# Kernel tuning notes

Measured on AMD Instinct MI355X. Metric: run time of the kernel, lower is better.

Reference implementation:

```python
import jax, jax.numpy as jnp
import numpy as np

MAX_RES = 5.0  # max_residue_magnitude
DG = 16       # deform_groups
KH = KW = 3
K = KH * KW
PAD = 1
STRIDE = 1
DIL = 1


def conv3x3(x, w, b):
    y = jax.lax.conv_general_dilated(
        x, w, window_strides=(1, 1), padding='SAME',
        dimension_numbers=('NCHW', 'OIHW', 'NCHW'))
    return y + b[None, :, None, None]


def lrelu(x):
    return jnp.where(x >= 0, x, 0.1 * x)


def deform_conv2d(x, offset, mask, weight, bias):
    # x: [B,C,H,W]; offset: [B,2*DG*K,Ho,Wo]; mask: [B,DG*K,Ho,Wo]
    B, C, H, W = x.shape
    Cout = weight.shape[0]
    Ho = (H + 2 * PAD - DIL * (KH - 1) - 1) // STRIDE + 1
    Wo = (W + 2 * PAD - DIL * (KW - 1) - 1) // STRIDE + 1
    Cg = C // DG

    # torchvision layout: offset channel = g*(2*K) + 2*k + {0:y, 1:x}
    off = offset.reshape(B, DG, K, 2, Ho, Wo)
    oy, ox = off[:, :, :, 0], off[:, :, :, 1]           # [B,DG,K,Ho,Wo]
    msk = mask.reshape(B, DG, K, Ho, Wo)

    ki = DIL * (jnp.arange(K) // KW)                    # [K] kernel row offsets
    kj = DIL * (jnp.arange(K) % KW)
    base_y = STRIDE * jnp.arange(Ho) - PAD              # [Ho]
    base_x = STRIDE * jnp.arange(Wo) - PAD              # [Wo]
    py = base_y[None, None, None, :, None] + ki[None, None, :, None, None] + oy
    px = base_x[None, None, None, None, :] + kj[None, None, :, None, None] + ox

    xg = x.reshape(B, DG, Cg, H * W)

    y0 = jnp.floor(py)
    x0 = jnp.floor(px)
    wy1 = py - y0
    wx1 = px - x0

    def corner(iy, ix, w_c):
        valid = ((iy >= 0) & (iy <= H - 1) & (ix >= 0) & (ix <= W - 1)).astype(x.dtype)
        iyc = jnp.clip(iy, 0, H - 1).astype(jnp.int32)
        ixc = jnp.clip(ix, 0, W - 1).astype(jnp.int32)
        idx = (iyc * W + ixc).reshape(B, DG, 1, K * Ho * Wo)
        g = jnp.take_along_axis(
            xg, jnp.broadcast_to(idx, (B, DG, Cg, K * Ho * Wo)), axis=3)
        g = g.reshape(B, DG, Cg, K, Ho, Wo)
        return g * (w_c * valid)[:, :, None]

    val = (corner(y0, x0, (1 - wy1) * (1 - wx1))
           + corner(y0, x0 + 1, (1 - wy1) * wx1)
           + corner(y0 + 1, x0, wy1 * (1 - wx1))
           + corner(y0 + 1, x0 + 1, wy1 * wx1))

    val = val * msk[:, :, None]                          # modulation
    val = val.reshape(B, C, K, Ho, Wo)                   # columns
    out = jnp.einsum('bckhw,ock->bohw', val, weight.reshape(Cout, C, K))
    return out + bias[None, :, None, None]


def setup_inputs() -> dict:
    key = jax.random.key(0)
    ks = jax.random.split(key, 12)
    B, H, W = 1, 192, 192
    inp = {
        'x':    jax.random.normal(ks[0], (B, 128, H, W), jnp.float32),
        'cond': jax.random.normal(ks[1], (B, 192, H, W), jnp.float32),
        'weight': jax.random.normal(ks[2], (64, 128, 3, 3), jnp.float32) * 0.03,
        'bias':   jax.random.normal(ks[3], (64,), jnp.float32) * 0.01,
        'w1': jax.random.normal(ks[4], (64, 192, 3, 3), jnp.float32) * 0.03,
        'b1': jax.random.normal(ks[5], (64,), jnp.float32) * 0.01,
        'w2': jax.random.normal(ks[6], (64, 64, 3, 3), jnp.float32) * 0.05,
        'b2': jax.random.normal(ks[7], (64,), jnp.float32) * 0.01,
        'w3': jax.random.normal(ks[8], (64, 64, 3, 3), jnp.float32) * 0.05,
        'b3': jax.random.normal(ks[9], (64,), jnp.float32) * 0.01,
        'w4': jax.random.normal(ks[10], (432, 64, 3, 3), jnp.float32) * 0.05,
        'b4': jax.random.normal(ks[11], (432,), jnp.float32) * 0.01,
    }
    return inp


def reference(x, cond, weight, bias, w1, b1, w2, b2, w3, b3, w4, b4):
    h = lrelu(conv3x3(cond, w1, b1))
    h = lrelu(conv3x3(h, w2, b2))
    h = lrelu(conv3x3(h, w3, b3))
    out = conv3x3(h, w4, b4)                       # [B, 27*DG, H, W]
    offset, mask = out[:, :18 * DG], out[:, 18 * DG:]
    offset = MAX_RES * jnp.tanh(offset)
    mask = jax.nn.sigmoid(mask)
    return deform_conv2d(x, offset, mask, weight, bias)
```

## Files before the change

kernel.cpp:

```cpp
#include <hip/hip_runtime.h>
#include <hip/hip_bf16.h>
#include <math.h>

#define IMG_H 192
#define IMG_W 192
#define NPIX (IMG_H * IMG_W)
#define PADW 194
#define PPIX (PADW * PADW)
#define PH 208
#define PW 208

typedef _Float16 h8 __attribute__((ext_vector_type(8)));
typedef _Float16 h4 __attribute__((ext_vector_type(4)));
typedef float f32x4 __attribute__((ext_vector_type(4)));

__device__ __forceinline__ float act_tanh5(float x) {
    const float t = __expf(2.f * x);
    return 5.f * (t - 1.f) / (t + 1.f);
}
__device__ __forceinline__ float act_sig(float x) {
    return 1.f / (1.f + __expf(-x));
}

typedef __attribute__((address_space(1))) const unsigned int GU32;
typedef __attribute__((address_space(3))) unsigned int LU32;
__device__ __forceinline__ void cp16(const void* g, void* l) {
    __builtin_amdgcn_global_load_lds((GU32*)g, (LU32*)l, 16, 0, 0);
}

__global__ __launch_bounds__(256) void cond_pack_k(
    const float* __restrict__ src, _Float16* __restrict__ dst)
{
    const int y = blockIdx.x;
    const int c = blockIdx.y;
    const int x = threadIdx.x;
    if (x >= PADW) return;
    const bool inb = (y >= 1 && y <= IMG_H && x >= 1 && x <= IMG_W);
    h8 v[4];
#pragma unroll
    for (int j = 0; j < 32; j++)
        ((_Float16*)v)[j] = inb
            ? (_Float16)src[(size_t)(c * 32 + j) * NPIX + (y - 1) * IMG_W + (x - 1)]
            : (_Float16)0.f;
    h8* d = (h8*)&dst[((size_t)c * PPIX + (size_t)y * PADW + x) * 32];
    d[0] = v[0]; d[1] = v[1]; d[2] = v[2]; d[3] = v[3];
}

template<int CIN, int COP, int COUT>
__device__ __forceinline__ void pack_body(
    int bx, const float* __restrict__ src, _Float16* __restrict__ dst)
{
    const int chunk = bx / 9, k = bx % 9;
    for (int i = threadIdx.x; i < COP * 32; i += 256) {
        const int co = i >> 5, cil = i & 31;
        float v = 0.f;
        if (co < COUT)
            v = src[((size_t)(co * CIN + chunk * 32 + cil)) * 9 + k];
        dst[(size_t)bx * COP * 32 + i] = (_Float16)v;
    }
}

__global__ __launch_bounds__(256) void pack_all_w_k(
    const float* __restrict__ w1, const float* __restrict__ w2,
    const float* __restrict__ w3, const float* __restrict__ w4,
    _Float16* __restrict__ wp1, _Float16* __restrict__ wp2,
    _Float16* __restrict__ wp3, _Float16* __restrict__ wp4)
{
    const int b = blockIdx.x;
    if      (b < 54) pack_body<192, 64, 64>(b, w1, wp1);
    else if (b < 72) pack_body<64, 64, 64>(b - 54, w2, wp2);
    else if (b < 90) pack_body<64, 64, 64>(b - 72, w3, wp3);
    else             pack_body<64, 448, 432>(b - 90, w4, wp4);
}

__global__ __launch_bounds__(192) void xg_pack_k(
    const float* __restrict__ x, _Float16* __restrict__ xg)
{
    const int y  = blockIdx.x;
    const int dg = blockIdx.y;
    const int xc = threadIdx.x;
    h8 v;
#pragma unroll
    for (int chl = 0; chl < 8; chl++)
        v[chl] = (_Float16)x[(size_t)(dg * 8 + chl) * NPIX + y * IMG_W + xc];
    *(h8*)&xg[(((size_t)dg * PH + y + 6) * PW + xc + 6) * 8] = v;
}

__global__ __launch_bounds__(256) void wdg_pack_k(
    const float* __restrict__ w, _Float16* __restrict__ wdg)
{
    const int i = blockIdx.x * 256 + threadIdx.x;
    if (i >= 16 * 64 * 96) return;
    const int ks = i % 96;
    const int rest = i / 96;
    const int co = rest % 64;
    const int dg = rest / 64;
    const int k = ks >> 3, chl = ks & 7;
    float v = 0.f;
    if (ks < 72)
        v = w[((size_t)co * 128 + dg * 8 + chl) * 9 + k];
    wdg[i] = (_Float16)v;
}

template<int CHUNKS, int ACT, int COP, int T8>
__global__ __launch_bounds__(256) void conv_lds_k(
    const _Float16* __restrict__ in,
    const _Float16* __restrict__ wpk,
    const float* __restrict__ bias,
    _Float16* __restrict__ out)
{
    constexpr int HALO = T8 ? 10 : 18;
    constexpr int NF   = T8 ? 1 : 4;
    constexpr int TDIM = T8 ? 24 : 12;
    constexpr int TSZ  = T8 ? 8 : 16;
    constexpr int INU  = HALO * HALO * 4;
    constexpr int ROWU = HALO * 4;

    __shared__ _Float16 in_lds[HALO * HALO * 32];
    __shared__ _Float16 w_lds[9 * 64 * 32];

    const int t    = threadIdx.x;
    const int lane = t & 63;
    const int wv   = __builtin_amdgcn_readfirstlane(t >> 6);
    const int col  = lane & 15;
    const int quad = lane >> 4;
    const int bx   = blockIdx.x;
    const int tx0  = (bx % TDIM) * TSZ;
    const int ty0  = (bx / TDIM) * TSZ;
    const int cobase = blockIdx.y * 64;

    f32x4 acc[4][NF];
#pragma unroll
    for (int m = 0; m < 4; m++)
#pragma unroll
        for (int s = 0; s < NF; s++) {
            f32x4 z = {0.f, 0.f, 0.f, 0.f};
            acc[m][s] = z;
        }

    for (int c = 0; c < CHUNKS; c++) {
        __syncthreads();
        {
            const char* gbase = (const char*)in + (size_t)c * PPIX * 64;
            char* lbase = (char*)in_lds + (size_t)wv * 64 * 16;
#pragma unroll
            for (int i = 0; i < (INU + 255) / 256; i++) {
                const int j = t + i * 256;
                if (j < INU) {
                    const int row = j / ROWU;
                    const int u   = j - row * ROWU;
                    cp16(gbase + ((size_t)(ty0 + row) * PADW + tx0) * 64 + u * 16,
                         lbase + (size_t)i * 256 * 16);
                }
            }
        }
        {
            const char* gw = (const char*)wpk
                + ((size_t)(c * 9) * COP + cobase) * 64 + t * 16;
            char* lw = (char*)w_lds + (size_t)wv * 64 * 16;
#pragma unroll
            for (int k = 0; k < 9; k++)
                cp16(gw + (size_t)k * COP * 64, lw + k * 4096);
        }
        __syncthreads();

#pragma unroll
        for (int k = 0; k < 9; k++) {
            const int ky = k / 3, kx = k % 3;
            h8 af[4];
#pragma unroll
            for (int m = 0; m < 4; m++)
                af[m] = *(const h8*)&w_lds[(k * 64 + m * 16 + col) * 32 + quad * 8];
            h8 bf[NF];
            if (T8) {
                bf[0] = *(const h8*)&in_lds[
                    ((2 * wv + (col >> 3) + ky) * HALO + (col & 7) + kx) * 32 + quad * 8];
            } else {
#pragma unroll
                for (int s = 0; s < NF; s++)
                    bf[s] = *(const h8*)&in_lds[
                        ((4 * wv + s + ky) * HALO + col + kx) * 32 + quad * 8];
            }
#pragma unroll
            for (int m = 0; m < 4; m++)
#pragma unroll
                for (int s = 0; s < NF; s++)
                    acc[m][s] = __builtin_amdgcn_mfma_f32_16x16x32_f16(
                        af[m], bf[s], acc[m][s], 0, 0, 0);
        }
    }

#pragma unroll
    for (int m = 0; m < 4; m++) {
#pragma unroll
        for (int s = 0; s < NF; s++) {
            int gy, gx;
            if (T8) { gy = ty0 + 2 * wv + (col >> 3); gx = tx0 + (col & 7); }
            else    { gy = ty0 + 4 * wv + s;          gx = tx0 + col; }
            const int ca = cobase + m * 16 + quad * 4;
            if (ACT == 1) {
                h4 st;
#pragma unroll
                for (int r = 0; r < 4; r++) {
                    float v = acc[m][s][r] + bias[ca + r];
                    st[r] = (_Float16)((v >= 0.f) ? v : 0.1f * v);
                }
                *(h4*)&out[((size_t)(ca >> 5) * PPIX + (size_t)(gy + 1) * PADW + (gx + 1)) * 32
                           + (ca & 31)] = st;
            } else {
#pragma unroll
                for (int r = 0; r < 4; r++) {
                    const int co = ca + r;
                    if (co < 432)
                        out[(size_t)co * NPIX + (size_t)gy * IMG_W + gx] =
                            (_Float16)(acc[m][s][r] + bias[co]);
                }
            }
        }
    }
}

__global__ __launch_bounds__(256) void deform_mfma_k(
    const _Float16* __restrict__ xg,
    const _Float16* __restrict__ od,
    const _Float16* __restrict__ wdg,
    const float* __restrict__ bias,
    float* __restrict__ out)
{
    __shared__ __align__(16) _Float16 val4[4][32][104];

    const int t    = threadIdx.x;
    const int lane = t & 63;
    const int wv   = __builtin_amdgcn_readfirstlane(t >> 6);
    const int col  = lane & 15;
    const int quad = lane >> 4;
    const int bx   = blockIdx.x;
    const int gy   = bx / 6;
    const int gx0  = (bx % 6) * 32;
    const int pixrow = gy * IMG_W + gx0;

    for (int i = t; i < 4 * 32 * 4; i += 256) {
        const int dgl = i >> 7;
        const int r   = i & 127;
        const int px  = r >> 2;
        const int j   = r & 3;
        h8 z = {0, 0, 0, 0, 0, 0, 0, 0};
        *(h8*)&val4[dgl][px][72 + 8 * j] = z;
    }

    f32x4 acc[2];
    {
        f32x4 z = {0.f, 0.f, 0.f, 0.f};
        acc[0] = z; acc[1] = z;
    }

    for (int dq = 0; dq < 4; dq++) {
        __syncthreads();
        for (int idx = t; idx < 1152; idx += 256) {
            const int pxl  = idx & 31;
            const int rest = idx >> 5;
            const int k    = rest % 9;
            const int dgl  = rest / 9;
            const int dg   = dq * 4 + dgl;
            const int kc   = dg * 9 + k;
            const int pix  = pixrow + pxl;
            const float oy = act_tanh5((float)od[(size_t)(2 * kc) * NPIX + pix]);
            const float ox = act_tanh5((float)od[(size_t)(2 * kc + 1) * NPIX + pix]);
            const float m  = act_sig((float)od[(size_t)(288 + kc) * NPIX + pix]);
            const float py  = (float)(gy - 1 + k / 3) + oy;
            const float pxx = (float)(gx0 + pxl - 1 + k % 3) + ox;
            const float y0 = floorf(py), x0 = floorf(pxx);
            const float fy = py - y0, fx = pxx - x0;
            const int iy = (int)y0 + 6, ix = (int)x0 + 6;
            const _Float16* p = xg + (((size_t)dg * PH + iy) * PW + ix) * 8;
            const h8 c00 = *(const h8*)p;
            const h8 c01 = *(const h8*)(p + 8);
            const h8 c10 = *(const h8*)(p + PW * 8);
            const h8 c11 = *(const h8*)(p + PW * 8 + 8);
            const float ey = 1.f - fy, ex = 1.f - fx;
            const _Float16 s00 = (_Float16)(ey * ex * m);
            const _Float16 s01 = (_Float16)(ey * fx * m);
            const _Float16 s10 = (_Float16)(fy * ex * m);
            const _Float16 s11 = (_Float16)(fy * fx * m);
            const h8 v = c00 * s00 + c01 * s01 + c10 * s10 + c11 * s11;
            *(h8*)&val4[dgl][pxl][k * 8] = v;
        }
        __syncthreads();

#pragma unroll
        for (int dgl = 0; dgl < 4; dgl++) {
            const int dg = dq * 4 + dgl;
            const _Float16* wbase = wdg + ((size_t)dg * 64 + wv * 16 + col) * 96;
#pragma unroll
            for (int ks = 0; ks < 3; ks++) {
                const h8 a  = *(const h8*)(wbase + ks * 32 + quad * 8);
                const h8 b0 = *(const h8*)&val4[dgl][col][ks * 32 + quad * 8];
                const h8 b1 = *(const h8*)&val4[dgl][16 + col][ks * 32 + quad * 8];
                acc[0] = __builtin_amdgcn_mfma_f32_16x16x32_f16(a, b0, acc[0], 0, 0, 0);
                acc[1] = __builtin_amdgcn_mfma_f32_16x16x32_f16(a, b1, acc[1], 0, 0, 0);
            }
        }
    }

    const int co = wv * 16 + quad * 4;
#pragma unroll
    for (int n = 0; n < 2; n++) {
        const int gx = gx0 + n * 16 + col;
#pragma unroll
        for (int r = 0; r < 4; r++)
            out[(size_t)(co + r) * NPIX + gy * IMG_W + gx] = acc[n][r] + bias[co + r];
    }
}

extern "C" void kernel_launch(void* const* d_in, const int* in_sizes, int n_in,
                              void* d_out, int out_size, void* d_ws, size_t ws_size,
                              hipStream_t stream) {
    (void)in_sizes; (void)n_in; (void)out_size; (void)ws_size;

    const float* x      = (const float*)d_in[0];
    const float* cond   = (const float*)d_in[1];
    const float* weight = (const float*)d_in[2];
    const float* bias   = (const float*)d_in[3];
    const float* w1     = (const float*)d_in[4];
    const float* b1     = (const float*)d_in[5];
    const float* w2     = (const float*)d_in[6];
    const float* b2     = (const float*)d_in[7];
    const float* w3     = (const float*)d_in[8];
    const float* b3     = (const float*)d_in[9];
    const float* w4     = (const float*)d_in[10];
    const float* b4     = (const float*)d_in[11];
    float* out = (float*)d_out;

    char* ws = (char*)d_ws;
    size_t off = 0;
    auto take = [&](size_t bytes) -> char* {
        char* p = ws + off;
        off = (off + bytes + 255) & ~(size_t)255;
        return p;
    };
    _Float16* act_cond = (_Float16*)take((size_t)6 * PPIX * 32 * 2);
    _Float16* pb_all   = (_Float16*)take((size_t)3 * 2 * PPIX * 32 * 2);
    _Float16* pb1 = pb_all;
    _Float16* pb2 = pb1 + (size_t)2 * PPIX * 32;
    _Float16* pb3 = pb2 + (size_t)2 * PPIX * 32;
    _Float16* od  = (_Float16*)take((size_t)432 * NPIX * 2);
    _Float16* wp1 = (_Float16*)take((size_t)54 * 64 * 32 * 2);
    _Float16* wp2 = (_Float16*)take((size_t)18 * 64 * 32 * 2);
    _Float16* wp3 = (_Float16*)take((size_t)18 * 64 * 32 * 2);
    _Float16* wp4 = (_Float16*)take((size_t)18 * 448 * 32 * 2);
    _Float16* xg  = (_Float16*)take((size_t)16 * PH * PW * 8 * 2);
    _Float16* wdg = (_Float16*)take((size_t)16 * 64 * 96 * 2);

    hipMemsetAsync(pb_all, 0, (size_t)3 * 2 * PPIX * 32 * 2, stream);
    hipMemsetAsync(xg,     0, (size_t)16 * PH * PW * 8 * 2, stream);

    hipLaunchKernelGGL(cond_pack_k, dim3(PADW, 6), dim3(256), 0, stream, cond, act_cond);
    hipLaunchKernelGGL(pack_all_w_k, dim3(108), dim3(256), 0, stream,
                       w1, w2, w3, w4, wp1, wp2, wp3, wp4);
    hipLaunchKernelGGL(xg_pack_k,  dim3(192, 16), dim3(192), 0, stream, x, xg);
    hipLaunchKernelGGL(wdg_pack_k, dim3((16 * 64 * 96 + 255) / 256), dim3(256), 0, stream, weight, wdg);

    hipLaunchKernelGGL((conv_lds_k<6, 1, 64, 1>),  dim3(576, 1), dim3(256), 0, stream, act_cond, wp1, b1, pb1);
    hipLaunchKernelGGL((conv_lds_k<2, 1, 64, 1>),  dim3(576, 1), dim3(256), 0, stream, pb1, wp2, b2, pb2);
    hipLaunchKernelGGL((conv_lds_k<2, 1, 64, 1>),  dim3(576, 1), dim3(256), 0, stream, pb2, wp3, b3, pb3);
    hipLaunchKernelGGL((conv_lds_k<2, 2, 448, 0>), dim3(144, 7), dim3(256), 0, stream, pb3, wp4, b4, od);
    hipLaunchKernelGGL(deform_mfma_k, dim3(1152), dim3(256), 0, stream, xg, od, wdg, bias, out);
}
```

Baseline: 259.6 us.

## Batch deform sampling into two 8-group chunks with staged loads for memory-level parallelism

The deformable-conv kernel now handles 8 deform groups per chunk (2 chunks instead of 4), doubling the shared val buffer. The sampling loop is split into three fully unrolled phases: issue all offset/mask loads, compute the bilinear coordinates, then issue all corner gathers. This exposes more outstanding memory requests per thread and halves the number of barriers. The cost is more registers and LDS, partly bounded by launch_bounds(256,3), with a risk of spills or lower occupancy.

```diff
diff --git a/kernel.cpp b/kernel.cpp
--- a/kernel.cpp
+++ b/kernel.cpp
@@ -220,14 +220,14 @@
     }
 }
 
-__global__ __launch_bounds__(256) void deform_mfma_k(
+__global__ __launch_bounds__(256, 3) void deform_mfma_k(
     const _Float16* __restrict__ xg,
     const _Float16* __restrict__ od,
     const _Float16* __restrict__ wdg,
     const float* __restrict__ bias,
     float* __restrict__ out)
 {
-    __shared__ __align__(16) _Float16 val4[4][32][104];
+    __shared__ __align__(16) _Float16 val4[8][32][104];
 
     const int t    = threadIdx.x;
     const int lane = t & 63;
@@ -239,7 +239,7 @@
     const int gx0  = (bx % 6) * 32;
     const int pixrow = gy * IMG_W + gx0;
 
-    for (int i = t; i < 4 * 32 * 4; i += 256) {
+    for (int i = t; i < 8 * 32 * 4; i += 256) {
         const int dgl = i >> 7;
         const int r   = i & 127;
         const int px  = r >> 2;
@@ -254,42 +254,71 @@
         acc[0] = z; acc[1] = z;
     }
 
-    for (int dq = 0; dq < 4; dq++) {
+    for (int ch = 0; ch < 2; ch++) {
         __syncthreads();
-        for (int idx = t; idx < 1152; idx += 256) {
-            const int pxl  = idx & 31;
-            const int rest = idx >> 5;
+
+        _Float16 ry[9], rx[9], rm[9];
+#pragma unroll
+        for (int u = 0; u < 9; u++) {
+            const int id   = t + (u << 8);
+            const int pxl  = id & 31;
+            const int rest = id >> 5;
             const int k    = rest % 9;
             const int dgl  = rest / 9;
-            const int dg   = dq * 4 + dgl;
-            const int kc   = dg * 9 + k;
+            const int kc   = (ch * 8 + dgl) * 9 + k;
             const int pix  = pixrow + pxl;
-            const float oy = act_tanh5((float)od[(size_t)(2 * kc) * NPIX + pix]);
-            const float ox = act_tanh5((float)od[(size_t)(2 * kc + 1) * NPIX + pix]);
-            const float m  = act_sig((float)od[(size_t)(288 + kc) * NPIX + pix]);
+            ry[u] = od[(size_t)(2 * kc) * NPIX + pix];
+            rx[u] = od[(size_t)(2 * kc + 1) * NPIX + pix];
+            rm[u] = od[(size_t)(288 + kc) * NPIX + pix];
+        }
+
+        int   goff[9];
+        float fy[9], fx[9], fm[9];
+#pragma unroll
+        for (int u = 0; u < 9; u++) {
+            const int id   = t + (u << 8);
+            const int pxl  = id & 31;
+            const int rest = id >> 5;
+            const int k    = rest % 9;
+            const int dgl  = rest / 9;
+            const int dg   = ch * 8 + dgl;
+            const float oy = act_tanh5((float)ry[u]);
+            const float ox = act_tanh5((float)rx[u]);
+            fm[u] = act_sig((float)rm[u]);
             const float py  = (float)(gy - 1 + k / 3) + oy;
             const float pxx = (float)(gx0 + pxl - 1 + k % 3) + ox;
             const float y0 = floorf(py), x0 = floorf(pxx);
-            const float fy = py - y0, fx = pxx - x0;
+            fy[u] = py - y0;
+            fx[u] = pxx - x0;
             const int iy = (int)y0 + 6, ix = (int)x0 + 6;
-            const _Float16* p = xg + (((size_t)dg * PH + iy) * PW + ix) * 8;
+            goff[u] = ((dg * PH + iy) * PW + ix) * 8;
+        }
+
+#pragma unroll
+        for (int u = 0; u < 9; u++) {
+            const int id   = t + (u << 8);
+            const int pxl  = id & 31;
+            const int rest = id >> 5;
+            const int k    = rest % 9;
+            const int dgl  = rest / 9;
+            const _Float16* p = xg + goff[u];
             const h8 c00 = *(const h8*)p;
             const h8 c01 = *(const h8*)(p + 8);
             const h8 c10 = *(const h8*)(p + PW * 8);
             const h8 c11 = *(const h8*)(p + PW * 8 + 8);
-            const float ey = 1.f - fy, ex = 1.f - fx;
-            const _Float16 s00 = (_Float16)(ey * ex * m);
-            const _Float16 s01 = (_Float16)(ey * fx * m);
-            const _Float16 s10 = (_Float16)(fy * ex * m);
-            const _Float16 s11 = (_Float16)(fy * fx * m);
+            const float ey = 1.f - fy[u], ex = 1.f - fx[u];
+            const _Float16 s00 = (_Float16)(ey * ex * fm[u]);
+            const _Float16 s01 = (_Float16)(ey * fx[u] * fm[u]);
+            const _Float16 s10 = (_Float16)(fy[u] * ex * fm[u]);
+            const _Float16 s11 = (_Float16)(fy[u] * fx[u] * fm[u]);
             const h8 v = c00 * s00 + c01 * s01 + c10 * s10 + c11 * s11;
             *(h8*)&val4[dgl][pxl][k * 8] = v;
         }
         __syncthreads();
 
 #pragma unroll
-        for (int dgl = 0; dgl < 4; dgl++) {
-            const int dg = dq * 4 + dgl;
+        for (int dgl = 0; dgl < 8; dgl++) {
+            const int dg = ch * 8 + dgl;
             const _Float16* wbase = wdg + ((size_t)dg * 64 + wv * 16 + col) * 96;
 #pragma unroll
             for (int ks = 0; ks < 3; ks++) {
```

New measurement: 267.5 us. +3.0%, slower.

## Store offset conv output in pixel-tiled layout and stage it into LDS

Applied to the files above, without the earlier changes.

The final offset/mask conv now writes its 432-channel output in a [pixel-block of 32][channel][32] layout, so each deform block's offsets sit in one contiguous region. The deform kernel copies that region into a new LDS buffer with 16-byte async copies (cp16) per channel quarter, then reads offsets and masks from LDS. This replaces scattered strided global loads of 64-byte rows with coalesced bulk copies. The cost is an extra barrier per iteration and more shared memory, and the conv epilogue's stores become more scattered.

```diff
diff --git a/kernel.cpp b/kernel.cpp
--- a/kernel.cpp
+++ b/kernel.cpp
@@ -211,9 +211,11 @@
 #pragma unroll
                 for (int r = 0; r < 4; r++) {
                     const int co = ca + r;
-                    if (co < 432)
-                        out[(size_t)co * NPIX + (size_t)gy * IMG_W + gx] =
+                    if (co < 432) {
+                        const int pix = gy * IMG_W + gx;
+                        out[((size_t)(pix >> 5) * 432 + co) * 32 + (pix & 31)] =
                             (_Float16)(acc[m][s][r] + bias[co]);
+                    }
                 }
             }
         }
@@ -228,6 +230,7 @@
     float* __restrict__ out)
 {
     __shared__ __align__(16) _Float16 val4[4][32][104];
+    __shared__ __align__(16) _Float16 od_lds[108 * 32];
 
     const int t    = threadIdx.x;
     const int lane = t & 63;
@@ -237,7 +240,6 @@
     const int bx   = blockIdx.x;
     const int gy   = bx / 6;
     const int gx0  = (bx % 6) * 32;
-    const int pixrow = gy * IMG_W + gx0;
 
     for (int i = t; i < 4 * 32 * 4; i += 256) {
         const int dgl = i >> 7;
@@ -256,17 +258,33 @@
 
     for (int dq = 0; dq < 4; dq++) {
         __syncthreads();
+
+        {
+            const char* gA = (const char*)od + ((size_t)bx * 432 + dq * 72) * 64;
+            const char* gB = (const char*)od + ((size_t)bx * 432 + 288 + dq * 36) * 64;
+            char* lbase = (char*)od_lds + (size_t)wv * 64 * 16;
+#pragma unroll
+            for (int i = 0; i < 2; i++) {
+                const int j = t + i * 256;
+                if (j < 432) {
+                    const char* src = (j < 288) ? gA + (size_t)j * 16
+                                                : gB + (size_t)(j - 288) * 16;
+                    cp16(src, lbase + (size_t)i * 256 * 16);
+                }
+            }
+        }
+        __syncthreads();
+
         for (int idx = t; idx < 1152; idx += 256) {
             const int pxl  = idx & 31;
             const int rest = idx >> 5;
             const int k    = rest % 9;
             const int dgl  = rest / 9;
             const int dg   = dq * 4 + dgl;
-            const int kc   = dg * 9 + k;
-            const int pix  = pixrow + pxl;
-            const float oy = act_tanh5((float)od[(size_t)(2 * kc) * NPIX + pix]);
-            const float ox = act_tanh5((float)od[(size_t)(2 * kc + 1) * NPIX + pix]);
-            const float m  = act_sig((float)od[(size_t)(288 + kc) * NPIX + pix]);
+            const int rA   = 2 * (dgl * 9 + k);
+            const float oy = act_tanh5((float)od_lds[rA * 32 + pxl]);
+            const float ox = act_tanh5((float)od_lds[(rA + 1) * 32 + pxl]);
+            const float m  = act_sig((float)od_lds[(72 + dgl * 9 + k) * 32 + pxl]);
             const float py  = (float)(gy - 1 + k / 3) + oy;
             const float pxx = (float)(gx0 + pxl - 1 + k % 3) + ox;
             const float y0 = floorf(py), x0 = floorf(pxx);
```

Result: slower. 266.4 us (+2.6%).
